# Optimization experiments

Measured on AMD Instinct MI355X. Metric: run time of the kernel, lower is better.

Reference implementation:

```python
import jax, jax.numpy as jnp
import numpy as np

N = 96        # num_nodes
D = 64        # emb_size / n_hid
BS = 16
T = 13
G = 1         # num_graph

# all N^2 ordered pairs, receiver-major: edge e=i*N+j has receiver i, sender j
_REC = jnp.repeat(jnp.arange(N), N)
_SEND = jnp.tile(jnp.arange(N), N)


def _lin(shape, key, scale=0.05):
    return (jax.random.normal(key, shape, dtype=jnp.float32) * scale)


def setup_inputs() -> dict:
    key = jax.random.key(0)
    ks = jax.random.split(key, 24)
    inp = {
        "skill_seq": jax.random.randint(ks[0], (BS, T), 0, N, dtype=jnp.int32),
        "adj": jax.random.uniform(ks[1], (G, BS, N, N), dtype=jnp.float32),
        "node_embeddings": jax.random.normal(ks[2], (G, N, D), dtype=jnp.float32),
        # edge MLP
        "W_msg1": _lin((2 * D, D), ks[3]), "b_msg1": jnp.zeros((D,), jnp.float32),
        "W_msg2": _lin((D, D), ks[4]),     "b_msg2": jnp.zeros((D,), jnp.float32),
        # GRU hidden projections (no bias)
        "W_hr": _lin((D, D), ks[5]), "W_hi": _lin((D, D), ks[6]), "W_hh": _lin((D, D), ks[7]),
        # GRU input projections (bias)
        "W_ir": _lin((D, D), ks[8]),  "b_ir": jnp.zeros((D,), jnp.float32),
        "W_ii": _lin((D, D), ks[9]),  "b_ii": jnp.zeros((D,), jnp.float32),
        "W_in": _lin((D, D), ks[10]), "b_in": jnp.zeros((D,), jnp.float32),
        # output MLP
        "W_o1": _lin((D, D), ks[11]), "b_o1": jnp.zeros((D,), jnp.float32),
        "W_o2": _lin((D, D), ks[12]), "b_o2": jnp.zeros((D,), jnp.float32),
        "W_o3": _lin((D, D), ks[13]), "b_o3": jnp.zeros((D,), jnp.float32),
    }
    return inp


def _forward(skill_seq, adj, node_embeddings,
             W_msg1, b_msg1, W_msg2, b_msg2,
             W_hr, W_hi, W_hh,
             W_ir, b_ir, W_ii, b_ii, W_in, b_in,
             W_o1, b_o1, W_o2, b_o2, W_o3, b_o3):
    bs, time_steps = skill_seq.shape
    hidden0 = jnp.zeros((G, bs, N, D), dtype=adj.dtype)
    emb = node_embeddings[0]  # [N, D] (num_graph=1)

    def step(hidden, skill_t):
        # gather senders/receivers over the node axis -> [G, bs, N^2, 2D]
        senders = hidden[:, :, _SEND, :]
        receivers = hidden[:, :, _REC, :]
        pre_msg = jnp.concatenate([senders, receivers], axis=-1)
        msg = jnp.tanh(pre_msg @ W_msg1 + b_msg1)        # [G, bs, N^2, D]
        msg = jnp.tanh(msg @ W_msg2 + b_msg2)
        msg = msg.reshape(G, bs, N, N, D)                # receiver i, sender j
        # mask by adjacency and scatter-sum over senders, then /N
        agg = jnp.einsum('gbij,gbijd->gbid', adj, msg) / N   # [G, bs, N, D]
        inputs = emb[skill_t][None, :, None, :]          # [1, bs, 1, D]
        r = jax.nn.sigmoid(inputs @ W_ir + b_ir + agg @ W_hr)
        i = jax.nn.sigmoid(inputs @ W_ii + b_ii + agg @ W_hi)
        n = jnp.tanh(inputs @ W_in + b_in + r * (agg @ W_hh))
        hidden = (1.0 - i) * n + i * hidden
        pred = jax.nn.relu(hidden @ W_o1 + b_o1)
        pred = jax.nn.relu(pred @ W_o2 + b_o2)
        pred = pred @ W_o3 + b_o3                        # [G, bs, N, D]
        return hidden, pred

    skills_t = skill_seq[:, :time_steps - 1].T           # [T-1, bs]
    _, preds = jax.lax.scan(step, hidden0, skills_t)     # [T-1, G, bs, N, D]
    # torch: stack(dim=1) -> [G, T-1, bs, N, D]; transpose(1,2) -> [G, bs, T-1, N, D]
    return jnp.transpose(preds, (1, 2, 0, 3, 4))


def reference(skill_seq, adj, node_embeddings,
              W_msg1, b_msg1, W_msg2, b_msg2,
              W_hr, W_hi, W_hh,
              W_ir, b_ir, W_ii, b_ii, W_in, b_in,
              W_o1, b_o1, W_o2, b_o2, W_o3, b_o3):
    return _forward(skill_seq, adj, node_embeddings,
                    W_msg1, b_msg1, W_msg2, b_msg2,
                    W_hr, W_hi, W_hh,
                    W_ir, b_ir, W_ii, b_ii, W_in, b_in,
                    W_o1, b_o1, W_o2, b_o2, W_o3, b_o3)
```

## Files before the change

kernel.cpp:

```cpp
#include <hip/hip_runtime.h>

typedef unsigned short ushort_t;
typedef __attribute__((ext_vector_type(8))) short short8;
typedef __attribute__((ext_vector_type(4))) float floatx4;

#define NN 96
#define DD 64
#define BSZ 16
#define TSTEP 12
#define JSPLIT 8
#define JPW 12
#define ITILES 6

#define OFF_HALL  0u
#define OFF_S     5111808u
#define OFF_R     5505024u
#define OFF_E     5898240u
#define OFF_PART  5971968u
#define OFF_WSWZ  9117696u
#define HSLOT     98304

static __device__ __forceinline__ short f2bf(float f){
    union { float f; unsigned u; } v; v.f = f;
    unsigned u = v.u;
    u += 0x7fffu + ((u >> 16) & 1u);
    return (short)(u >> 16);
}
static __device__ __forceinline__ float fast_tanh(float x){
    x = fminf(20.f, fmaxf(-20.f, x));
    float p = __expf(2.f * x);
    return (p - 1.f) * __builtin_amdgcn_rcpf(p + 1.f);
}
static __device__ __forceinline__ float fast_sigmoid(float x){
    x = fminf(30.f, fmaxf(-30.f, x));
    float p = __expf(-x);
    return __builtin_amdgcn_rcpf(1.f + p);
}
static __device__ __forceinline__ void zero4(floatx4* a){
    floatx4 z = {0.f,0.f,0.f,0.f};
    a[0]=z; a[1]=z; a[2]=z; a[3]=z;
}
static __device__ __forceinline__ void buildA(const float* sM, int col, int quad, short8& a0, short8& a1){
    floatx4 f0 = *(const floatx4*)&sM[col*68 + quad*8];
    floatx4 f1 = *(const floatx4*)&sM[col*68 + quad*8 + 4];
    floatx4 f2 = *(const floatx4*)&sM[col*68 + 32 + quad*8];
    floatx4 f3 = *(const floatx4*)&sM[col*68 + 32 + quad*8 + 4];
    #pragma unroll
    for (int jj = 0; jj < 4; jj++){
        a0[jj]   = f2bf(f0[jj]);
        a0[4+jj] = f2bf(f1[jj]);
        a1[jj]   = f2bf(f2[jj]);
        a1[4+jj] = f2bf(f3[jj]);
    }
}
static __device__ __forceinline__ void mm16(short8 a0, short8 a1, const short8* wzm, int l, floatx4* acc){
    #pragma unroll
    for (int nt = 0; nt < 4; nt++){
        short8 b0 = wzm[nt*64 + l];
        short8 b1 = wzm[(4 + nt)*64 + l];
        acc[nt] = __builtin_amdgcn_mfma_f32_16x16x32_bf16(a0, b0, acc[nt], 0, 0, 0);
        acc[nt] = __builtin_amdgcn_mfma_f32_16x16x32_bf16(a1, b1, acc[nt], 0, 0, 0);
    }
}
static __device__ __forceinline__ void mm16r(short8 a0, short8 a1, const short8* f, floatx4* acc){
    #pragma unroll
    for (int nt = 0; nt < 4; nt++){
        acc[nt] = __builtin_amdgcn_mfma_f32_16x16x32_bf16(a0, f[nt],     acc[nt], 0, 0, 0);
        acc[nt] = __builtin_amdgcn_mfma_f32_16x16x32_bf16(a1, f[4 + nt], acc[nt], 0, 0, 0);
    }
}

__global__ __launch_bounds__(256) void k_init(
    const float* __restrict__ emb, const float* __restrict__ Wmsg1,
    const float* __restrict__ Wmsg2,
    const float* __restrict__ Whr, const float* __restrict__ Whi, const float* __restrict__ Whh,
    const float* __restrict__ Wir, const float* __restrict__ bir,
    const float* __restrict__ Wii, const float* __restrict__ bii,
    const float* __restrict__ Win, const float* __restrict__ bin,
    const float* __restrict__ Wo1, const float* __restrict__ Wo2, const float* __restrict__ Wo3,
    float* __restrict__ hz, float* __restrict__ SRz,
    float* __restrict__ Ef, ushort_t* __restrict__ wswz)
{
    int wg = blockIdx.x, tid = threadIdx.x;
    if (wg < 288) {
        int flat = wg*256 + tid;
        floatx4 z = {0.f,0.f,0.f,0.f};
        if (flat < 24576) ((floatx4*)hz)[flat] = z;
        else              ((floatx4*)SRz)[flat - 24576] = z;
    } else if (wg < 360) {
        int flat = (wg - 288)*256 + tid;
        int m = flat / 6144; int r = flat % 6144; int s = r >> 6; int d = r & 63;
        const float* W = (m==0)? Wir : (m==1)? Wii : Win;
        const float* B = (m==0)? bir : (m==1)? bii : bin;
        float acc = B[d];
        #pragma unroll 8
        for (int k = 0; k < 64; k++)
            acc += emb[s*64 + k] * W[k*64 + d];
        Ef[flat] = acc;
    } else {
        int flat = (wg - 360)*256 + tid;
        int m = flat >> 12; int q = flat & 4095;
        int jj = q & 7, lane = (q >> 3) & 63, nt = (q >> 9) & 3, kc = q >> 11;
        int k = kc*32 + ((lane >> 4) << 3) + jj;
        int n = nt*16 + (lane & 15);
        const float* src; int idx = k*64 + n;
        switch (m) {
          case 0: src = Wmsg2; break;
          case 1: src = Whr;  break;
          case 2: src = Whi;  break;
          case 3: src = Whh;  break;
          case 4: src = Wmsg1; break;
          case 5: src = Wmsg1; idx = (64 + k)*64 + n; break;
          case 6: src = Wo1; break;
          case 7: src = Wo2; break;
          default: src = Wo3; break;
        }
        wswz[flat] = (ushort_t)f2bf(src[idx]);
    }
}

__global__ __launch_bounds__(256) void k_msg(
    const float* __restrict__ adj, const float* __restrict__ b1in, const float* __restrict__ b2in,
    const float* __restrict__ Sg, const float* __restrict__ Rg,
    const ushort_t* __restrict__ wswz, float* __restrict__ partial)
{
    __shared__ float sS[JPW*64];
    __shared__ float sRB[16*68];
    __shared__ float sAdj[16*JPW];
    __shared__ float sAgg[4][16*68];
    int wg = blockIdx.x;
    int js = wg / 96; int rem = wg % 96; int b = rem / 6; int it = rem % 6;
    int tid = threadIdx.x; int w = tid >> 6; int l = tid & 63;
    int quad = l >> 4, col = l & 15;
    int j0 = js * JPW;

    for (int q = tid; q < JPW*16; q += 256) {
        int row = q >> 4, c4 = (q & 15) * 4;
        *(floatx4*)&sS[row*64 + c4] = *(const floatx4*)&Sg[(b*NN + j0 + row)*64 + c4];
    }
    for (int q = tid; q < 16*16; q += 256) {
        int row = q >> 4, c4 = (q & 15) * 4;
        floatx4 r4 = *(const floatx4*)&Rg[(b*NN + it*16 + row)*64 + c4];
        floatx4 b4 = *(const floatx4*)&b1in[c4];
        floatx4 o = r4 + b4;
        *(floatx4*)&sRB[row*68 + c4] = o;
    }
    for (int q = tid; q < 16*JPW; q += 256) {
        int i = q / JPW, j = q % JPW;
        sAdj[q] = adj[(b*NN + it*16 + i)*NN + j0 + j];
    }
    const short8* wz = (const short8*)wswz;
    short8 w2f[2][4];
    #pragma unroll
    for (int kc = 0; kc < 2; kc++)
      #pragma unroll
      for (int nt = 0; nt < 4; nt++)
        w2f[kc][nt] = wz[(kc*4 + nt)*64 + l];
    float b2v[4];
    #pragma unroll
    for (int nt = 0; nt < 4; nt++) b2v[nt] = b2in[nt*16 + col];
    __syncthreads();

    float rbv[16];
    #pragma unroll
    for (int c = 0; c < 4; c++)
        *(floatx4*)&rbv[c*4] = *(const floatx4*)&sRB[col*68 + (c>>1)*32 + quad*8 + (c&1)*4];

    float agg[4][4];
    #pragma unroll
    for (int nt=0;nt<4;nt++)
      #pragma unroll
      for (int r=0;r<4;r++) agg[nt][r] = 0.f;

    for (int c = 0; c < 3; c++) {
        int jl = w*3 + c;
        float sv[16];
        #pragma unroll
        for (int cc = 0; cc < 4; cc++)
            *(floatx4*)&sv[cc*4] = *(const floatx4*)&sS[jl*64 + (cc>>1)*32 + quad*8 + (cc&1)*4];
        short8 a0, a1;
        #pragma unroll
        for (int e = 0; e < 8; e++) {
            a0[e] = f2bf(fast_tanh(sv[e]   + rbv[e]));
            a1[e] = f2bf(fast_tanh(sv[8+e] + rbv[8+e]));
        }
        floatx4 acc[4];
        zero4(acc);
        #pragma unroll
        for (int nt = 0; nt < 4; nt++) {
            acc[nt] = __builtin_amdgcn_mfma_f32_16x16x32_bf16(a0, w2f[0][nt], acc[nt], 0,0,0);
            acc[nt] = __builtin_amdgcn_mfma_f32_16x16x32_bf16(a1, w2f[1][nt], acc[nt], 0,0,0);
        }
        float adjv[4];
        #pragma unroll
        for (int r = 0; r < 4; r++) adjv[r] = sAdj[(quad*4 + r)*JPW + jl];
        #pragma unroll
        for (int nt = 0; nt < 4; nt++)
          #pragma unroll
          for (int r = 0; r < 4; r++)
            agg[nt][r] += adjv[r] * fast_tanh(acc[nt][r] + b2v[nt]);
    }
    #pragma unroll
    for (int nt = 0; nt < 4; nt++)
      #pragma unroll
      for (int r = 0; r < 4; r++)
        sAgg[w][(quad*4 + r)*68 + nt*16 + col] = agg[nt][r];
    __syncthreads();
    {
        int i = tid >> 4, k4 = (tid & 15) * 4;
        floatx4 s0 = *(const floatx4*)&sAgg[0][i*68 + k4];
        floatx4 s1 = *(const floatx4*)&sAgg[1][i*68 + k4];
        floatx4 s2 = *(const floatx4*)&sAgg[2][i*68 + k4];
        floatx4 s3 = *(const floatx4*)&sAgg[3][i*68 + k4];
        floatx4 o = (s0 + s1) + (s2 + s3);
        o = o * (1.f/96.f);
        *(floatx4*)&partial[((js*BSZ + b)*NN + it*16 + i)*64 + k4] = o;
    }
}

__global__ __launch_bounds__(256) void k_gru(
    const int* __restrict__ skills, const float* __restrict__ partial,
    const float* __restrict__ Ef, const ushort_t* __restrict__ wswz,
    const float* __restrict__ hprev, float* __restrict__ hcur,
    float* __restrict__ Sg, float* __restrict__ Rg, int t)
{
    __shared__ float sM[16*68];
    __shared__ float sG[3][16*68];
    __shared__ float sH[16*64];
    __shared__ float sE[3][64];
    int wg = blockIdx.x; int b = wg / 6, it = wg % 6;
    int tid = threadIdx.x; int w = tid >> 6; int l = tid & 63;
    int quad = l >> 4, col = l & 15;
    int i = tid >> 4, k4 = (tid & 15) * 4;

    const short8* wzb = (const short8*)wswz;
    short8 fG[8], fSR[8];
    if (w < 3) {
        #pragma unroll
        for (int q = 0; q < 8; q++) fG[q] = wzb[(1 + w)*512 + q*64 + l];
    }
    if (w < 2) {
        #pragma unroll
        for (int q = 0; q < 8; q++) fSR[q] = wzb[(4 + w)*512 + q*64 + l];
    }

    {
        floatx4 a = {0.f,0.f,0.f,0.f};
        #pragma unroll
        for (int p = 0; p < JSPLIT; p++)
            a += *(const floatx4*)&partial[((p*BSZ + b)*NN + it*16 + i)*64 + k4];
        *(floatx4*)&sM[i*68 + k4] = a;
        *(floatx4*)&sH[i*64 + k4] = *(const floatx4*)&hprev[(b*NN + it*16 + i)*64 + k4];
    }
    if (tid < 192) {
        int s = skills[b*13 + t];
        ((float*)sE)[tid] = Ef[(tid >> 6)*6144 + s*64 + (tid & 63)];
    }
    __syncthreads();

    if (w < 3) {
        short8 a0, a1;
        buildA(sM, col, quad, a0, a1);
        floatx4 acc[4];
        zero4(acc);
        mm16r(a0, a1, fG, acc);
        #pragma unroll
        for (int nt = 0; nt < 4; nt++)
          #pragma unroll
          for (int r = 0; r < 4; r++)
            sG[w][(quad*4 + r)*68 + nt*16 + col] = acc[nt][r];
    }
    __syncthreads();

    {
        float h[4];
        #pragma unroll
        for (int e = 0; e < 4; e++) {
            int d = k4 + e;
            float gr = fast_sigmoid(sE[0][d] + sG[0][i*68 + d]);
            float gi = fast_sigmoid(sE[1][d] + sG[1][i*68 + d]);
            float nv = fast_tanh(sE[2][d] + gr * sG[2][i*68 + d]);
            h[e] = (1.f - gi)*nv + gi*sH[i*64 + d];
        }
        #pragma unroll
        for (int e = 0; e < 4; e++) sM[i*68 + k4 + e] = h[e];
        floatx4 hv = { h[0], h[1], h[2], h[3] };
        *(floatx4*)&hcur[(b*NN + it*16 + i)*64 + k4] = hv;
    }
    __syncthreads();

    if (w < 2) {
        short8 a0, a1;
        buildA(sM, col, quad, a0, a1);
        floatx4 acc[4];
        zero4(acc);
        mm16r(a0, a1, fSR, acc);
        float* dst = (w == 0) ? Sg : Rg;
        #pragma unroll
        for (int nt = 0; nt < 4; nt++)
          #pragma unroll
          for (int r = 0; r < 4; r++)
            dst[(b*NN + it*16 + quad*4 + r)*64 + nt*16 + col] = acc[nt][r];
    }
}

__global__ __launch_bounds__(256) void k_out(
    const float* __restrict__ hall, const ushort_t* __restrict__ wswz,
    const float* __restrict__ bo1, const float* __restrict__ bo2, const float* __restrict__ bo3,
    float* __restrict__ out)
{
    __shared__ float sT[4][16*68];
    int tid = threadIdx.x; int w = tid >> 6; int l = tid & 63;
    int quad = l >> 4, col = l & 15;
    int g = blockIdx.x*4 + w;
    int ts = g / 96; int rem = g % 96; int b = rem / 6, it = rem % 6;
    const float* hsrc = hall + (size_t)(ts + 1)*HSLOT + (b*NN + it*16)*64;
    float* sm = sT[w];
    {
        int i = l >> 2, c0 = (l & 3) * 16;
        #pragma unroll
        for (int cc = 0; cc < 4; cc++)
            *(floatx4*)&sm[i*68 + c0 + cc*4] = *(const floatx4*)&hsrc[i*64 + c0 + cc*4];
    }
    float bv1[4], bv2[4], bv3[4];
    #pragma unroll
    for (int nt = 0; nt < 4; nt++) {
        bv1[nt] = bo1[nt*16 + col];
        bv2[nt] = bo2[nt*16 + col];
        bv3[nt] = bo3[nt*16 + col];
    }
    short8 a0, a1;
    floatx4 acc[4];

    buildA(sm, col, quad, a0, a1);
    zero4(acc);
    mm16(a0, a1, (const short8*)wswz + 6*512, l, acc);
    #pragma unroll
    for (int nt = 0; nt < 4; nt++)
      #pragma unroll
      for (int r = 0; r < 4; r++)
        sm[(quad*4 + r)*68 + nt*16 + col] = fmaxf(0.f, acc[nt][r] + bv1[nt]);

    buildA(sm, col, quad, a0, a1);
    zero4(acc);
    mm16(a0, a1, (const short8*)wswz + 7*512, l, acc);
    #pragma unroll
    for (int nt = 0; nt < 4; nt++)
      #pragma unroll
      for (int r = 0; r < 4; r++)
        sm[(quad*4 + r)*68 + nt*16 + col] = fmaxf(0.f, acc[nt][r] + bv2[nt]);

    buildA(sm, col, quad, a0, a1);
    zero4(acc);
    mm16(a0, a1, (const short8*)wswz + 8*512, l, acc);
    #pragma unroll
    for (int nt = 0; nt < 4; nt++)
      #pragma unroll
      for (int r = 0; r < 4; r++)
        out[((b*TSTEP + ts)*NN + it*16 + quad*4 + r)*64 + nt*16 + col] = acc[nt][r] + bv3[nt];
}

extern "C" void kernel_launch(void* const* d_in, const int* in_sizes, int n_in,
                              void* d_out, int out_size, void* d_ws, size_t ws_size,
                              hipStream_t stream) {
    const int*   skills = (const int*)d_in[0];
    const float* adj    = (const float*)d_in[1];
    const float* emb    = (const float*)d_in[2];
    const float* Wmsg1  = (const float*)d_in[3];
    const float* b1     = (const float*)d_in[4];
    const float* Wmsg2  = (const float*)d_in[5];
    const float* b2     = (const float*)d_in[6];
    const float* Whr    = (const float*)d_in[7];
    const float* Whi    = (const float*)d_in[8];
    const float* Whh    = (const float*)d_in[9];
    const float* Wir    = (const float*)d_in[10];
    const float* bir    = (const float*)d_in[11];
    const float* Wii    = (const float*)d_in[12];
    const float* bii    = (const float*)d_in[13];
    const float* Win    = (const float*)d_in[14];
    const float* bin    = (const float*)d_in[15];
    const float* Wo1    = (const float*)d_in[16];
    const float* bo1    = (const float*)d_in[17];
    const float* Wo2    = (const float*)d_in[18];
    const float* bo2    = (const float*)d_in[19];
    const float* Wo3    = (const float*)d_in[20];
    const float* bo3    = (const float*)d_in[21];

    char* ws = (char*)d_ws;
    float*    hall    = (float*)(ws + OFF_HALL);
    float*    Sg      = (float*)(ws + OFF_S);
    float*    Rg      = (float*)(ws + OFF_R);
    float*    Ef      = (float*)(ws + OFF_E);
    float*    partial = (float*)(ws + OFF_PART);
    ushort_t* wswz    = (ushort_t*)(ws + OFF_WSWZ);
    float*    out     = (float*)d_out;

    k_init<<<dim3(504), dim3(256), 0, stream>>>(emb, Wmsg1, Wmsg2, Whr, Whi, Whh,
        Wir, bir, Wii, bii, Win, bin, Wo1, Wo2, Wo3, hall, Sg, Ef, wswz);

    for (int t = 0; t < TSTEP; t++) {
        k_msg<<<dim3(JSPLIT*BSZ*ITILES), dim3(256), 0, stream>>>(adj, b1, b2, Sg, Rg, wswz, partial);
        k_gru<<<dim3(BSZ*ITILES), dim3(256), 0, stream>>>(skills, partial, Ef, wswz,
            hall + (size_t)t*HSLOT, hall + (size_t)(t+1)*HSLOT, Sg, Rg, t);
    }
    k_out<<<dim3(288), dim3(256), 0, stream>>>(hall, wswz, bo1, bo2, bo3, out);
}
```

Measured before the change: 273.5 us.

## Fuse message and GRU kernels via last-block atomic counter

Merges the per-step message kernel and GRU kernel into one launch. The last of the JSPLIT workgroups for each (batch, tile) detects completion through an atomic counter and runs the GRU update. S/R buffers are double-buffered so that workgroups still reading the previous step's S/R do not race with writers. This halves the number of kernel launches per step, at the cost of threadfences, atomics, and serialized tail work done by a few blocks.

Result: slower. 978.6 us (+257.9%).

```diff
diff --git a/kernel.cpp b/kernel.cpp
--- a/kernel.cpp
+++ b/kernel.cpp
@@ -13,11 +13,14 @@
 #define ITILES 6
 
 #define OFF_HALL  0u
-#define OFF_S     5111808u
-#define OFF_R     5505024u
-#define OFF_E     5898240u
-#define OFF_PART  5971968u
-#define OFF_WSWZ  9117696u
+#define OFF_S0    5111808u
+#define OFF_S1    5505024u
+#define OFF_R0    5898240u
+#define OFF_R1    6291456u
+#define OFF_E     6684672u
+#define OFF_PART  6758400u
+#define OFF_WSWZ  9904128u
+#define OFF_CNT   9977856u
 #define HSLOT     98304
 
 static __device__ __forceinline__ short f2bf(float f){
@@ -78,15 +81,21 @@
     const float* __restrict__ Wii, const float* __restrict__ bii,
     const float* __restrict__ Win, const float* __restrict__ bin,
     const float* __restrict__ Wo1, const float* __restrict__ Wo2, const float* __restrict__ Wo3,
-    float* __restrict__ hz, float* __restrict__ SRz,
+    float* __restrict__ hz, float* __restrict__ S0, float* __restrict__ R0,
+    int* __restrict__ cnt,
     float* __restrict__ Ef, ushort_t* __restrict__ wswz)
 {
     int wg = blockIdx.x, tid = threadIdx.x;
     if (wg < 288) {
         int flat = wg*256 + tid;
         floatx4 z = {0.f,0.f,0.f,0.f};
-        if (flat < 24576) ((floatx4*)hz)[flat] = z;
-        else              ((floatx4*)SRz)[flat - 24576] = z;
+        if      (flat < 24576) ((floatx4*)hz)[flat] = z;
+        else if (flat < 49152) ((floatx4*)S0)[flat - 24576] = z;
+        else                   ((floatx4*)R0)[flat - 49152] = z;
+        if (wg < 5) {
+            int c = wg*256 + tid;
+            if (c < TSTEP*BSZ*ITILES) cnt[c] = 0;
+        }
     } else if (wg < 360) {
         int flat = (wg - 288)*256 + tid;
         int m = flat / 6144; int r = flat % 6144; int s = r >> 6; int d = r & 63;
@@ -119,15 +128,22 @@
     }
 }
 
-__global__ __launch_bounds__(256) void k_msg(
+__global__ __launch_bounds__(256) void k_step(
     const float* __restrict__ adj, const float* __restrict__ b1in, const float* __restrict__ b2in,
-    const float* __restrict__ Sg, const float* __restrict__ Rg,
-    const ushort_t* __restrict__ wswz, float* __restrict__ partial)
+    const float* __restrict__ Sread, const float* __restrict__ Rread,
+    const ushort_t* __restrict__ wswz, float* __restrict__ partial,
+    const int* __restrict__ skills, const float* __restrict__ Ef,
+    const float* __restrict__ hprev, float* __restrict__ hcur,
+    float* __restrict__ Swrite, float* __restrict__ Rwrite,
+    int* __restrict__ cnt, int t)
 {
-    __shared__ float sS[JPW*64];
-    __shared__ float sRB[16*68];
-    __shared__ float sAdj[16*JPW];
-    __shared__ float sAgg[4][16*68];
+    __shared__ float lds[6400];
+    __shared__ int sLast;
+    float* sS   = lds;
+    float* sRB  = lds + 768;
+    float* sAdj = lds + 1856;
+    float* sAgg = lds + 2048;
+
     int wg = blockIdx.x;
     int js = wg / 96; int rem = wg % 96; int b = rem / 6; int it = rem % 6;
     int tid = threadIdx.x; int w = tid >> 6; int l = tid & 63;
@@ -136,11 +152,11 @@
 
     for (int q = tid; q < JPW*16; q += 256) {
         int row = q >> 4, c4 = (q & 15) * 4;
-        *(floatx4*)&sS[row*64 + c4] = *(const floatx4*)&Sg[(b*NN + j0 + row)*64 + c4];
+        *(floatx4*)&sS[row*64 + c4] = *(const floatx4*)&Sread[(b*NN + j0 + row)*64 + c4];
     }
     for (int q = tid; q < 16*16; q += 256) {
         int row = q >> 4, c4 = (q & 15) * 4;
-        floatx4 r4 = *(const floatx4*)&Rg[(b*NN + it*16 + row)*64 + c4];
+        floatx4 r4 = *(const floatx4*)&Rread[(b*NN + it*16 + row)*64 + c4];
         floatx4 b4 = *(const floatx4*)&b1in[c4];
         floatx4 o = r4 + b4;
         *(floatx4*)&sRB[row*68 + c4] = o;
@@ -204,34 +220,32 @@
     for (int nt = 0; nt < 4; nt++)
       #pragma unroll
       for (int r = 0; r < 4; r++)
-        sAgg[w][(quad*4 + r)*68 + nt*16 + col] = agg[nt][r];
+        sAgg[w*1088 + (quad*4 + r)*68 + nt*16 + col] = agg[nt][r];
     __syncthreads();
     {
         int i = tid >> 4, k4 = (tid & 15) * 4;
-        floatx4 s0 = *(const floatx4*)&sAgg[0][i*68 + k4];
-        floatx4 s1 = *(const floatx4*)&sAgg[1][i*68 + k4];
-        floatx4 s2 = *(const floatx4*)&sAgg[2][i*68 + k4];
-        floatx4 s3 = *(const floatx4*)&sAgg[3][i*68 + k4];
+        floatx4 s0 = *(const floatx4*)&sAgg[0*1088 + i*68 + k4];
+        floatx4 s1 = *(const floatx4*)&sAgg[1*1088 + i*68 + k4];
+        floatx4 s2 = *(const floatx4*)&sAgg[2*1088 + i*68 + k4];
+        floatx4 s3 = *(const floatx4*)&sAgg[3*1088 + i*68 + k4];
         floatx4 o = (s0 + s1) + (s2 + s3);
         o = o * (1.f/96.f);
         *(floatx4*)&partial[((js*BSZ + b)*NN + it*16 + i)*64 + k4] = o;
     }
-}
-
-__global__ __launch_bounds__(256) void k_gru(
-    const int* __restrict__ skills, const float* __restrict__ partial,
-    const float* __restrict__ Ef, const ushort_t* __restrict__ wswz,
-    const float* __restrict__ hprev, float* __restrict__ hcur,
-    float* __restrict__ Sg, float* __restrict__ Rg, int t)
-{
-    __shared__ float sM[16*68];
-    __shared__ float sG[3][16*68];
-    __shared__ float sH[16*64];
-    __shared__ float sE[3][64];
-    int wg = blockIdx.x; int b = wg / 6, it = wg % 6;
-    int tid = threadIdx.x; int w = tid >> 6; int l = tid & 63;
-    int quad = l >> 4, col = l & 15;
-    int i = tid >> 4, k4 = (tid & 15) * 4;
+
+    __threadfence();
+    if (tid == 0) {
+        int old = atomicAdd(&cnt[(t*BSZ*ITILES) + b*ITILES + it], 1);
+        sLast = (old == JSPLIT - 1);
+    }
+    __syncthreads();
+    if (!sLast) return;
+    __threadfence();
+
+    float* sM = lds;
+    float* sG = lds + 1088;
+    float* sH = lds + 4352;
+    float* sE = lds + 5376;
 
     const short8* wzb = (const short8*)wswz;
     short8 fG[8], fSR[8];
@@ -244,6 +258,7 @@
         for (int q = 0; q < 8; q++) fSR[q] = wzb[(4 + w)*512 + q*64 + l];
     }
 
+    int i = tid >> 4, k4 = (tid & 15) * 4;
     {
         floatx4 a = {0.f,0.f,0.f,0.f};
         #pragma unroll
@@ -254,7 +269,7 @@
     }
     if (tid < 192) {
         int s = skills[b*13 + t];
-        ((float*)sE)[tid] = Ef[(tid >> 6)*6144 + s*64 + (tid & 63)];
+        sE[tid] = Ef[(tid >> 6)*6144 + s*64 + (tid & 63)];
     }
     __syncthreads();
 
@@ -268,7 +283,7 @@
         for (int nt = 0; nt < 4; nt++)
           #pragma unroll
           for (int r = 0; r < 4; r++)
-            sG[w][(quad*4 + r)*68 + nt*16 + col] = acc[nt][r];
+            sG[w*1088 + (quad*4 + r)*68 + nt*16 + col] = acc[nt][r];
     }
     __syncthreads();
 
@@ -277,9 +292,9 @@
         #pragma unroll
         for (int e = 0; e < 4; e++) {
             int d = k4 + e;
-            float gr = fast_sigmoid(sE[0][d] + sG[0][i*68 + d]);
-            float gi = fast_sigmoid(sE[1][d] + sG[1][i*68 + d]);
-            float nv = fast_tanh(sE[2][d] + gr * sG[2][i*68 + d]);
+            float gr = fast_sigmoid(sE[d]       + sG[0*1088 + i*68 + d]);
+            float gi = fast_sigmoid(sE[64 + d]  + sG[1*1088 + i*68 + d]);
+            float nv = fast_tanh  (sE[128 + d] + gr * sG[2*1088 + i*68 + d]);
             h[e] = (1.f - gi)*nv + gi*sH[i*64 + d];
         }
         #pragma unroll
@@ -295,7 +310,7 @@
         floatx4 acc[4];
         zero4(acc);
         mm16r(a0, a1, fSR, acc);
-        float* dst = (w == 0) ? Sg : Rg;
+        float* dst = (w == 0) ? Swrite : Rwrite;
         #pragma unroll
         for (int nt = 0; nt < 4; nt++)
           #pragma unroll
@@ -388,20 +403,28 @@
 
     char* ws = (char*)d_ws;
     float*    hall    = (float*)(ws + OFF_HALL);
-    float*    Sg      = (float*)(ws + OFF_S);
-    float*    Rg      = (float*)(ws + OFF_R);
+    float*    S0      = (float*)(ws + OFF_S0);
+    float*    S1      = (float*)(ws + OFF_S1);
+    float*    R0      = (float*)(ws + OFF_R0);
+    float*    R1      = (float*)(ws + OFF_R1);
     float*    Ef      = (float*)(ws + OFF_E);
     float*    partial = (float*)(ws + OFF_PART);
     ushort_t* wswz    = (ushort_t*)(ws + OFF_WSWZ);
+    int*      cnt     = (int*)(ws + OFF_CNT);
     float*    out     = (float*)d_out;
 
     k_init<<<dim3(504), dim3(256), 0, stream>>>(emb, Wmsg1, Wmsg2, Whr, Whi, Whh,
-        Wir, bir, Wii, bii, Win, bin, Wo1, Wo2, Wo3, hall, Sg, Ef, wswz);
+        Wir, bir, Wii, bii, Win, bin, Wo1, Wo2, Wo3, hall, S0, R0, cnt, Ef, wswz);
 
     for (int t = 0; t < TSTEP; t++) {
-        k_msg<<<dim3(JSPLIT*BSZ*ITILES), dim3(256), 0, stream>>>(adj, b1, b2, Sg, Rg, wswz, partial);
-        k_gru<<<dim3(BSZ*ITILES), dim3(256), 0, stream>>>(skills, partial, Ef, wswz,
-            hall + (size_t)t*HSLOT, hall + (size_t)(t+1)*HSLOT, Sg, Rg, t);
+        const float* Sr = (t & 1) ? S1 : S0;
+        const float* Rr = (t & 1) ? R1 : R0;
+        float*       Sw = (t & 1) ? S0 : S1;
+        float*       Rw = (t & 1) ? R0 : R1;
+        k_step<<<dim3(JSPLIT*BSZ*ITILES), dim3(256), 0, stream>>>(
+            adj, b1, b2, Sr, Rr, wswz, partial, skills, Ef,
+            hall + (size_t)t*HSLOT, hall + (size_t)(t+1)*HSLOT,
+            Sw, Rw, cnt, t);
     }
     k_out<<<dim3(288), dim3(256), 0, stream>>>(hall, wswz, bo1, bo2, bo3, out);
 }
```

## Fuse GRU update into message kernel with redundant per-block recompute and ping-pong partials

Applied to the files above, without the earlier changes.

Removes the separate per-step GRU kernel. Each message block now reduces the previous step's partial aggregates and recomputes the GRU update plus the sender/receiver projections for the tiles it needs, then runs the message computation. Partial buffers alternate between two slots, and a final small kernel finishes the last hidden update. This halves the number of launches in the time loop and drops the S/R global round-trip, at the cost of redundant GRU and projection work spread across the JSPLIT blocks.

Measured after the change: 336.6 us. 23.1% more time.

```diff
diff --git a/kernel.cpp b/kernel.cpp
--- a/kernel.cpp
+++ b/kernel.cpp
@@ -13,11 +13,10 @@
 #define ITILES 6
 
 #define OFF_HALL  0u
-#define OFF_S     5111808u
-#define OFF_R     5505024u
-#define OFF_E     5898240u
-#define OFF_PART  5971968u
-#define OFF_WSWZ  9117696u
+#define OFF_E     5111808u
+#define OFF_P0    5185536u
+#define OFF_P1    8331264u
+#define OFF_WSWZ  11476992u
 #define HSLOT     98304
 
 static __device__ __forceinline__ short f2bf(float f){
@@ -60,13 +59,6 @@
         short8 b1 = wzm[(4 + nt)*64 + l];
         acc[nt] = __builtin_amdgcn_mfma_f32_16x16x32_bf16(a0, b0, acc[nt], 0, 0, 0);
         acc[nt] = __builtin_amdgcn_mfma_f32_16x16x32_bf16(a1, b1, acc[nt], 0, 0, 0);
-    }
-}
-static __device__ __forceinline__ void mm16r(short8 a0, short8 a1, const short8* f, floatx4* acc){
-    #pragma unroll
-    for (int nt = 0; nt < 4; nt++){
-        acc[nt] = __builtin_amdgcn_mfma_f32_16x16x32_bf16(a0, f[nt],     acc[nt], 0, 0, 0);
-        acc[nt] = __builtin_amdgcn_mfma_f32_16x16x32_bf16(a1, f[4 + nt], acc[nt], 0, 0, 0);
     }
 }
 
@@ -78,17 +70,14 @@
     const float* __restrict__ Wii, const float* __restrict__ bii,
     const float* __restrict__ Win, const float* __restrict__ bin,
     const float* __restrict__ Wo1, const float* __restrict__ Wo2, const float* __restrict__ Wo3,
-    float* __restrict__ hz, float* __restrict__ SRz,
-    float* __restrict__ Ef, ushort_t* __restrict__ wswz)
+    float* __restrict__ hz, float* __restrict__ Ef, ushort_t* __restrict__ wswz)
 {
     int wg = blockIdx.x, tid = threadIdx.x;
-    if (wg < 288) {
-        int flat = wg*256 + tid;
+    if (wg < 96) {
         floatx4 z = {0.f,0.f,0.f,0.f};
-        if (flat < 24576) ((floatx4*)hz)[flat] = z;
-        else              ((floatx4*)SRz)[flat - 24576] = z;
-    } else if (wg < 360) {
-        int flat = (wg - 288)*256 + tid;
+        ((floatx4*)hz)[wg*256 + tid] = z;
+    } else if (wg < 168) {
+        int flat = (wg - 96)*256 + tid;
         int m = flat / 6144; int r = flat % 6144; int s = r >> 6; int d = r & 63;
         const float* W = (m==0)? Wir : (m==1)? Wii : Win;
         const float* B = (m==0)? bir : (m==1)? bii : bin;
@@ -98,7 +87,7 @@
             acc += emb[s*64 + k] * W[k*64 + d];
         Ef[flat] = acc;
     } else {
-        int flat = (wg - 360)*256 + tid;
+        int flat = (wg - 168)*256 + tid;
         int m = flat >> 12; int q = flat & 4095;
         int jj = q & 7, lane = (q >> 3) & 63, nt = (q >> 9) & 3, kc = q >> 11;
         int k = kc*32 + ((lane >> 4) << 3) + jj;
@@ -119,36 +108,113 @@
     }
 }
 
-__global__ __launch_bounds__(256) void k_msg(
+__global__ __launch_bounds__(256, 3) void k_fused(
     const float* __restrict__ adj, const float* __restrict__ b1in, const float* __restrict__ b2in,
-    const float* __restrict__ Sg, const float* __restrict__ Rg,
-    const ushort_t* __restrict__ wswz, float* __restrict__ partial)
+    const int* __restrict__ skills, const float* __restrict__ Ef,
+    const ushort_t* __restrict__ wswz,
+    const float* __restrict__ pread, float* __restrict__ pwrite,
+    const float* __restrict__ hprev, float* __restrict__ hcur, int t)
 {
-    __shared__ float sS[JPW*64];
-    __shared__ float sRB[16*68];
-    __shared__ float sAdj[16*JPW];
-    __shared__ float sAgg[4][16*68];
+    __shared__ float lds[9664];
+    float* sS   = lds;
+    float* sRB  = lds + 768;
+    float* sAdj = lds + 1856;
+    float* sAgg = lds + 2048;
+    float* sMw  = lds + 6400;
+
     int wg = blockIdx.x;
     int js = wg / 96; int rem = wg % 96; int b = rem / 6; int it = rem % 6;
     int tid = threadIdx.x; int w = tid >> 6; int l = tid & 63;
     int quad = l >> 4, col = l & 15;
     int j0 = js * JPW;
 
-    for (int q = tid; q < JPW*16; q += 256) {
-        int row = q >> 4, c4 = (q & 15) * 4;
-        *(floatx4*)&sS[row*64 + c4] = *(const floatx4*)&Sg[(b*NN + j0 + row)*64 + c4];
-    }
-    for (int q = tid; q < 16*16; q += 256) {
-        int row = q >> 4, c4 = (q & 15) * 4;
-        floatx4 r4 = *(const floatx4*)&Rg[(b*NN + it*16 + row)*64 + c4];
-        floatx4 b4 = *(const floatx4*)&b1in[c4];
-        floatx4 o = r4 + b4;
-        *(floatx4*)&sRB[row*68 + c4] = o;
-    }
-    for (int q = tid; q < 16*JPW; q += 256) {
-        int i = q / JPW, j = q % JPW;
-        sAdj[q] = adj[(b*NN + it*16 + i)*NN + j0 + j];
-    }
+    if (t == 0) {
+        for (int q = tid; q < JPW*64; q += 256) sS[q] = 0.f;
+        for (int q = tid; q < 16*64; q += 256) sRB[(q >> 6)*68 + (q & 63)] = b1in[q & 63];
+        for (int q = tid; q < 16*JPW; q += 256) {
+            int i = q / JPW, j = q % JPW;
+            sAdj[q] = adj[(b*NN + it*16 + i)*NN + j0 + j];
+        }
+        __syncthreads();
+    } else {
+        int jt0 = j0 >> 4, jt1 = (j0 + JPW - 1) >> 4;
+        int myTile = -1;
+        if      (w == 0) myTile = it;
+        else if (w == 1) myTile = jt0;
+        else if (w == 2 && jt1 != jt0) myTile = jt1;
+        float* sm = sMw + (w < 3 ? w : 0)*1088;
+
+        if (w == 3) {
+            for (int q = l; q < 16*JPW; q += 64) {
+                int i = q / JPW, j = q % JPW;
+                sAdj[q] = adj[(b*NN + it*16 + i)*NN + j0 + j];
+            }
+        }
+        if (myTile >= 0) {
+            int i = l >> 2, c16 = (l & 3)*16;
+            floatx4 a[4]; zero4(a);
+            for (int p = 0; p < JSPLIT; p++) {
+                const float* base = &pread[((p*BSZ + b)*NN + myTile*16 + i)*64 + c16];
+                #pragma unroll
+                for (int cc = 0; cc < 4; cc++) a[cc] += *(const floatx4*)&base[cc*4];
+            }
+            #pragma unroll
+            for (int cc = 0; cc < 4; cc++) *(floatx4*)&sm[i*68 + c16 + cc*4] = a[cc];
+        }
+        __syncthreads();
+        if (myTile >= 0) {
+            short8 a0, a1; buildA(sm, col, quad, a0, a1);
+            floatx4 Ar[4], Ai[4], Ah[4];
+            zero4(Ar); zero4(Ai); zero4(Ah);
+            mm16(a0, a1, (const short8*)wswz + 1*512, l, Ar);
+            mm16(a0, a1, (const short8*)wswz + 2*512, l, Ai);
+            mm16(a0, a1, (const short8*)wswz + 3*512, l, Ah);
+            int s = skills[b*13 + (t-1)];
+            #pragma unroll
+            for (int nt = 0; nt < 4; nt++) {
+                int d = nt*16 + col;
+                float er = Ef[0*6144 + s*64 + d];
+                float ei = Ef[1*6144 + s*64 + d];
+                float en = Ef[2*6144 + s*64 + d];
+                #pragma unroll
+                for (int r = 0; r < 4; r++) {
+                    int row = myTile*16 + quad*4 + r;
+                    float gr = fast_sigmoid(er + Ar[nt][r]);
+                    float gi = fast_sigmoid(ei + Ai[nt][r]);
+                    float nv = fast_tanh  (en + gr*Ah[nt][r]);
+                    float hold = hprev[(b*NN + row)*64 + d];
+                    float h = (1.f - gi)*nv + gi*hold;
+                    sm[(quad*4 + r)*68 + d] = h;
+                    if (w == 0 && js == 0) hcur[(b*NN + row)*64 + d] = h;
+                }
+            }
+        }
+        __syncthreads();
+        if (myTile >= 0) {
+            short8 a0, a1; buildA(sm, col, quad, a0, a1);
+            floatx4 acc[4]; zero4(acc);
+            if (w == 0) {
+                mm16(a0, a1, (const short8*)wswz + 5*512, l, acc);
+                #pragma unroll
+                for (int nt = 0; nt < 4; nt++)
+                  #pragma unroll
+                  for (int r = 0; r < 4; r++)
+                    sRB[(quad*4 + r)*68 + nt*16 + col] = acc[nt][r] + b1in[nt*16 + col];
+            } else {
+                mm16(a0, a1, (const short8*)wswz + 4*512, l, acc);
+                #pragma unroll
+                for (int nt = 0; nt < 4; nt++)
+                  #pragma unroll
+                  for (int r = 0; r < 4; r++) {
+                    int loc = myTile*16 + quad*4 + r - j0;
+                    if (loc >= 0 && loc < JPW)
+                        sS[loc*64 + nt*16 + col] = acc[nt][r];
+                  }
+            }
+        }
+        __syncthreads();
+    }
+
     const short8* wz = (const short8*)wswz;
     short8 w2f[2][4];
     #pragma unroll
@@ -159,7 +225,6 @@
     float b2v[4];
     #pragma unroll
     for (int nt = 0; nt < 4; nt++) b2v[nt] = b2in[nt*16 + col];
-    __syncthreads();
 
     float rbv[16];
     #pragma unroll
@@ -204,25 +269,24 @@
     for (int nt = 0; nt < 4; nt++)
       #pragma unroll
       for (int r = 0; r < 4; r++)
-        sAgg[w][(quad*4 + r)*68 + nt*16 + col] = agg[nt][r];
+        sAgg[w*1088 + (quad*4 + r)*68 + nt*16 + col] = agg[nt][r];
     __syncthreads();
     {
-        int i = tid >> 4, k4 = (tid & 15) * 4;
-        floatx4 s0 = *(const floatx4*)&sAgg[0][i*68 + k4];
-        floatx4 s1 = *(const floatx4*)&sAgg[1][i*68 + k4];
-        floatx4 s2 = *(const floatx4*)&sAgg[2][i*68 + k4];
-        floatx4 s3 = *(const floatx4*)&sAgg[3][i*68 + k4];
+        int i = tid >> 4, k4 = (tid & 15)*4;
+        floatx4 s0 = *(const floatx4*)&sAgg[0*1088 + i*68 + k4];
+        floatx4 s1 = *(const floatx4*)&sAgg[1*1088 + i*68 + k4];
+        floatx4 s2 = *(const floatx4*)&sAgg[2*1088 + i*68 + k4];
+        floatx4 s3 = *(const floatx4*)&sAgg[3*1088 + i*68 + k4];
         floatx4 o = (s0 + s1) + (s2 + s3);
         o = o * (1.f/96.f);
-        *(floatx4*)&partial[((js*BSZ + b)*NN + it*16 + i)*64 + k4] = o;
-    }
-}
-
-__global__ __launch_bounds__(256) void k_gru(
-    const int* __restrict__ skills, const float* __restrict__ partial,
+        *(floatx4*)&pwrite[((js*BSZ + b)*NN + it*16 + i)*64 + k4] = o;
+    }
+}
+
+__global__ __launch_bounds__(256) void k_last(
+    const int* __restrict__ skills, const float* __restrict__ pread,
     const float* __restrict__ Ef, const ushort_t* __restrict__ wswz,
-    const float* __restrict__ hprev, float* __restrict__ hcur,
-    float* __restrict__ Sg, float* __restrict__ Rg, int t)
+    const float* __restrict__ hprev, float* __restrict__ hcur, int t)
 {
     __shared__ float sM[16*68];
     __shared__ float sG[3][16*68];
@@ -231,24 +295,13 @@
     int wg = blockIdx.x; int b = wg / 6, it = wg % 6;
     int tid = threadIdx.x; int w = tid >> 6; int l = tid & 63;
     int quad = l >> 4, col = l & 15;
-    int i = tid >> 4, k4 = (tid & 15) * 4;
-
-    const short8* wzb = (const short8*)wswz;
-    short8 fG[8], fSR[8];
-    if (w < 3) {
-        #pragma unroll
-        for (int q = 0; q < 8; q++) fG[q] = wzb[(1 + w)*512 + q*64 + l];
-    }
-    if (w < 2) {
-        #pragma unroll
-        for (int q = 0; q < 8; q++) fSR[q] = wzb[(4 + w)*512 + q*64 + l];
-    }
+    int i = tid >> 4, k4 = (tid & 15)*4;
 
     {
         floatx4 a = {0.f,0.f,0.f,0.f};
         #pragma unroll
         for (int p = 0; p < JSPLIT; p++)
-            a += *(const floatx4*)&partial[((p*BSZ + b)*NN + it*16 + i)*64 + k4];
+            a += *(const floatx4*)&pread[((p*BSZ + b)*NN + it*16 + i)*64 + k4];
         *(floatx4*)&sM[i*68 + k4] = a;
         *(floatx4*)&sH[i*64 + k4] = *(const floatx4*)&hprev[(b*NN + it*16 + i)*64 + k4];
     }
@@ -263,7 +316,7 @@
         buildA(sM, col, quad, a0, a1);
         floatx4 acc[4];
         zero4(acc);
-        mm16r(a0, a1, fG, acc);
+        mm16(a0, a1, (const short8*)wswz + (1 + w)*512, l, acc);
         #pragma unroll
         for (int nt = 0; nt < 4; nt++)
           #pragma unroll
@@ -273,34 +326,14 @@
     __syncthreads();
 
     {
-        float h[4];
         #pragma unroll
         for (int e = 0; e < 4; e++) {
             int d = k4 + e;
             float gr = fast_sigmoid(sE[0][d] + sG[0][i*68 + d]);
             float gi = fast_sigmoid(sE[1][d] + sG[1][i*68 + d]);
-            float nv = fast_tanh(sE[2][d] + gr * sG[2][i*68 + d]);
-            h[e] = (1.f - gi)*nv + gi*sH[i*64 + d];
-        }
-        #pragma unroll
-        for (int e = 0; e < 4; e++) sM[i*68 + k4 + e] = h[e];
-        floatx4 hv = { h[0], h[1], h[2], h[3] };
-        *(floatx4*)&hcur[(b*NN + it*16 + i)*64 + k4] = hv;
-    }
-    __syncthreads();
-
-    if (w < 2) {
-        short8 a0, a1;
-        buildA(sM, col, quad, a0, a1);
-        floatx4 acc[4];
-        zero4(acc);
-        mm16r(a0, a1, fSR, acc);
-        float* dst = (w == 0) ? Sg : Rg;
-        #pragma unroll
-        for (int nt = 0; nt < 4; nt++)
-          #pragma unroll
-          for (int r = 0; r < 4; r++)
-            dst[(b*NN + it*16 + quad*4 + r)*64 + nt*16 + col] = acc[nt][r];
+            float nv = fast_tanh  (sE[2][d] + gr * sG[2][i*68 + d]);
+            hcur[(b*NN + it*16 + i)*64 + d] = (1.f - gi)*nv + gi*sH[i*64 + d];
+        }
     }
 }
 
@@ -317,7 +350,7 @@
     const float* hsrc = hall + (size_t)(ts + 1)*HSLOT + (b*NN + it*16)*64;
     float* sm = sT[w];
     {
-        int i = l >> 2, c0 = (l & 3) * 16;
+        int i = l >> 2, c0 = (l & 3)*16;
         #pragma unroll
         for (int cc = 0; cc < 4; cc++)
             *(floatx4*)&sm[i*68 + c0 + cc*4] = *(const floatx4*)&hsrc[i*64 + c0 + cc*4];
@@ -387,21 +420,24 @@
     const float* bo3    = (const float*)d_in[21];
 
     char* ws = (char*)d_ws;
-    float*    hall    = (float*)(ws + OFF_HALL);
-    float*    Sg      = (float*)(ws + OFF_S);
-    float*    Rg      = (float*)(ws + OFF_R);
-    float*    Ef      = (float*)(ws + OFF_E);
-    float*    partial = (float*)(ws + OFF_PART);
-    ushort_t* wswz    = (ushort_t*)(ws + OFF_WSWZ);
-    float*    out     = (float*)d_out;
-
-    k_init<<<dim3(504), dim3(256), 0, stream>>>(emb, Wmsg1, Wmsg2, Whr, Whi, Whh,
-        Wir, bir, Wii, bii, Win, bin, Wo1, Wo2, Wo3, hall, Sg, Ef, wswz);
+    float*    hall = (float*)(ws + OFF_HALL);
+    float*    Ef   = (float*)(ws + OFF_E);
+    float*    P0   = (float*)(ws + OFF_P0);
+    float*    P1   = (float*)(ws + OFF_P1);
+    ushort_t* wswz = (ushort_t*)(ws + OFF_WSWZ);
+    float*    out  = (float*)d_out;
+
+    k_init<<<dim3(312), dim3(256), 0, stream>>>(emb, Wmsg1, Wmsg2, Whr, Whi, Whh,
+        Wir, bir, Wii, bii, Win, bin, Wo1, Wo2, Wo3, hall, Ef, wswz);
 
     for (int t = 0; t < TSTEP; t++) {
-        k_msg<<<dim3(JSPLIT*BSZ*ITILES), dim3(256), 0, stream>>>(adj, b1, b2, Sg, Rg, wswz, partial);
-        k_gru<<<dim3(BSZ*ITILES), dim3(256), 0, stream>>>(skills, partial, Ef, wswz,
-            hall + (size_t)t*HSLOT, hall + (size_t)(t+1)*HSLOT, Sg, Rg, t);
-    }
+        float* pw = (t & 1) ? P1 : P0;
+        const float* pr = (t & 1) ? P0 : P1;
+        k_fused<<<dim3(JSPLIT*BSZ*ITILES), dim3(256), 0, stream>>>(
+            adj, b1, b2, skills, Ef, wswz, pr, pw,
+            hall + (size_t)(t > 0 ? t-1 : 0)*HSLOT, hall + (size_t)t*HSLOT, t);
+    }
+    k_last<<<dim3(96), dim3(256), 0, stream>>>(skills, P1, Ef, wswz,
+        hall + 11*(size_t)HSLOT, hall + 12*(size_t)HSLOT, 11);
     k_out<<<dim3(288), dim3(256), 0, stream>>>(hall, wswz, bo1, bo2, bo3, out);
 }
```
